# Kernel tuning notes

Hardware: AMD Instinct MI355X
Metric: run time of the kernel (lower is better)

The kernel has to match this reference:

```python
import jax, jax.numpy as jnp
import numpy as np

NUM_USERS = 100000
NUM_ITEMS = 50000
N_NODES = NUM_USERS + NUM_ITEMS
N_EDGES = 2_000_000
D = 64          # embedding_dim
HEADS = 4
F1 = D // HEADS  # per-head out dim of gat1
BATCH = 16384
NEG_SLOPE = 0.2  # PyG GATConv default negative_slope


def setup_inputs() -> dict:
    key = jax.random.key(0)
    ks = jax.random.split(key, 13)
    inp = {}
    inp["edge_index"] = jax.random.randint(ks[0], (2, N_EDGES), 0, N_NODES, dtype=jnp.int64)
    inp["batch_user_idx"] = jax.random.randint(ks[1], (BATCH,), 0, NUM_USERS, dtype=jnp.int64)
    inp["batch_item_idx"] = jax.random.randint(ks[2], (BATCH,), 0, NUM_ITEMS, dtype=jnp.int64)
    # Embedding tables (nn.init.normal_ std=0.01)
    inp["user_emb"] = 0.01 * jax.random.normal(ks[3], (NUM_USERS, D), dtype=jnp.float32)
    inp["item_emb"] = 0.01 * jax.random.normal(ks[4], (NUM_ITEMS, D), dtype=jnp.float32)
    # gat1: GATConv(64, 16, heads=4, concat=True)
    inp["W1"] = jax.random.normal(ks[5], (D, HEADS * F1), dtype=jnp.float32) / np.sqrt(D)
    inp["a_src1"] = jax.random.normal(ks[6], (HEADS, F1), dtype=jnp.float32) / np.sqrt(F1)
    inp["a_dst1"] = jax.random.normal(ks[7], (HEADS, F1), dtype=jnp.float32) / np.sqrt(F1)
    inp["b1"] = jnp.zeros((HEADS * F1,), dtype=jnp.float32)
    # gat2: GATConv(64, 64, heads=1)
    inp["W2"] = jax.random.normal(ks[8], (D, D), dtype=jnp.float32) / np.sqrt(D)
    inp["a_src2"] = jax.random.normal(ks[9], (1, D), dtype=jnp.float32) / np.sqrt(D)
    inp["a_dst2"] = jax.random.normal(ks[10], (1, D), dtype=jnp.float32) / np.sqrt(D)
    inp["b2"] = jnp.zeros((D,), dtype=jnp.float32)
    return inp


def _gat_conv(x, src, dst, W, a_src, a_dst, b, num_nodes):
    """PyG GATConv (eval mode, concat, self-loops already in src/dst)."""
    H, F = a_src.shape
    h = (x @ W).reshape(num_nodes, H, F)                 # [N,H,F]
    alpha_s = jnp.einsum('nhf,hf->nh', h, a_src)         # [N,H]
    alpha_d = jnp.einsum('nhf,hf->nh', h, a_dst)
    e = alpha_s[src] + alpha_d[dst]                      # [E,H]
    e = jax.nn.leaky_relu(e, NEG_SLOPE)
    # scatter-softmax over destination neighborhoods
    m = jax.ops.segment_max(e, dst, num_segments=num_nodes)   # [N,H]
    e = jnp.exp(e - m[dst])
    denom = jax.ops.segment_sum(e, dst, num_segments=num_nodes)
    alpha = e / denom[dst]                               # [E,H]
    msg = h[src] * alpha[:, :, None]                     # [E,H,F]
    agg = jax.ops.segment_sum(msg, dst, num_segments=num_nodes)  # [N,H,F]
    return agg.reshape(num_nodes, H * F) + b


def reference(user_emb, item_emb, W1, a_src1, a_dst1, b1,
              W2, a_src2, a_dst2, b2,
              edge_index, batch_user_idx, batch_item_idx):
    x = jnp.concatenate([user_emb, item_emb], axis=0)    # [N,D]
    n = x.shape[0]
    loop = jnp.arange(n, dtype=edge_index.dtype)          # add_self_loops=True
    src = jnp.concatenate([edge_index[0], loop])
    dst = jnp.concatenate([edge_index[1], loop])
    x = jax.nn.elu(_gat_conv(x, src, dst, W1, a_src1, a_dst1, b1, n))
    x = jax.nn.elu(_gat_conv(x, src, dst, W2, a_src2, a_dst2, b2, n))
    u = x[batch_user_idx]
    v = x[batch_item_idx + NUM_USERS]
    return jax.nn.sigmoid(jnp.sum(u * v, axis=1))        # [BATCH]
```

## Files before the change

kernel.cpp:

```cpp
#include <hip/hip_runtime.h>
#include <math.h>

#define SHIFT 8
#define NBMAX 1024
#define CAP   4096
#define TILE  4096
#define HSCALE 64.0f

typedef float v2f __attribute__((ext_vector_type(2)));
typedef short bf16x8 __attribute__((ext_vector_type(8)));
typedef float f32x4 __attribute__((ext_vector_type(4)));

__device__ __forceinline__ unsigned short f2bf(float f) {
    unsigned u = __float_as_uint(f);
    unsigned r = u + 0x7FFFu + ((u >> 16) & 1u);
    return (unsigned short)(r >> 16);
}
__device__ __forceinline__ unsigned pack2bf(float lo, float hi) {
    return (unsigned)f2bf(lo) | ((unsigned)f2bf(hi) << 16);
}
__device__ __forceinline__ float bflo(unsigned u) { return __uint_as_float(u << 16); }
__device__ __forceinline__ float bfhi(unsigned u) { return __uint_as_float(u & 0xFFFF0000u); }


__global__ void k_prep_w(const float* __restrict__ W1, const float* __restrict__ W2,
                         unsigned short* __restrict__ WT1, unsigned short* __restrict__ WT2,
                         unsigned* __restrict__ gcur, int NB) {
    int t = blockIdx.x * 256 + threadIdx.x;
    if (t < 4096) {
        int n = t & 63, k = t >> 6;
        WT1[n * 64 + k] = f2bf(W1[k * 64 + n]);
        WT2[n * 64 + k] = f2bf(W2[k * 64 + n]);
    }
    if (t < NB) gcur[t] = (unsigned)t * CAP;
}


__global__ __launch_bounds__(512) void k_partition(
    const int* __restrict__ src, const int* __restrict__ dst, int E,
    unsigned* __restrict__ gcur, unsigned* __restrict__ pairs, int NB) {
    __shared__ unsigned lh[NBMAX];
    __shared__ unsigned lcur[NBMAX];
    int t = threadIdx.x;
    for (int q = t; q < NB; q += 512) lh[q] = 0;
    __syncthreads();
    int base = blockIdx.x * TILE;
    int end = min(E, base + TILE);
    for (int i = base + t; i < end; i += 512)
        atomicAdd(&lh[((unsigned)dst[i]) >> SHIFT], 1u);
    __syncthreads();
    for (int q = t; q < NB; q += 512) {
        unsigned c = lh[q];
        lcur[q] = c ? atomicAdd(&gcur[q], c) : 0u;
    }
    __syncthreads();
    for (int i = base + t; i < end; i += 512) {
        unsigned d = (unsigned)dst[i];
        unsigned pos = atomicAdd(&lcur[d >> SHIFT], 1u);
        pairs[pos] = ((d & 255u) << 18) | (unsigned)src[i];
    }
}

__global__ __launch_bounds__(512) void k_bucket_sort(
    const unsigned* __restrict__ pairs, const unsigned* __restrict__ gcur,
    unsigned* __restrict__ beg, unsigned* __restrict__ endd,
    int* __restrict__ srt, int N, int NB) {
    __shared__ unsigned lh[256];
    __shared__ unsigned lcur[256];
    __shared__ unsigned sh[256];
    __shared__ int ssrt[CAP];
    int b = blockIdx.x;
    int t = threadIdx.x;
    unsigned s0 = (unsigned)b * CAP;
    int cnt = (int)(gcur[b] - s0);
    if (t < 256) lh[t] = 0;
    __syncthreads();
    for (int i = t; i < cnt; i += 512)
        atomicAdd(&lh[pairs[s0 + i] >> 18], 1u);
    __syncthreads();
    unsigned deg_t = 0;
    if (t < 256) { deg_t = lh[t]; sh[t] = deg_t; }
    __syncthreads();
    for (int off = 1; off < 256; off <<= 1) {
        unsigned x = 0;
        if (t < 256 && t >= off) x = sh[t - off];
        __syncthreads();
        if (t < 256) sh[t] += x;
        __syncthreads();
    }
    if (t < 256) {
        unsigned excl = sh[t] - deg_t;
        lcur[t] = excl;
        int node = (b << SHIFT) + t;
        if (node < N) { beg[node] = s0 + excl; endd[node] = s0 + excl + deg_t; }
    }
    __syncthreads();
    for (int i = t; i < cnt; i += 512) {
        unsigned pk = pairs[s0 + i];
        unsigned p = atomicAdd(&lcur[pk >> 18], 1u);
        ssrt[p] = (int)(pk & 0x3FFFFu);
    }
    __syncthreads();
    for (int i = t; i < cnt; i += 512) srt[s0 + i] = ssrt[i];
}


template <int HT, int BIN>
__global__ __launch_bounds__(256) void k_linear_mfma(
    const void* __restrict__ xav, const void* __restrict__ xbv, int split,
    const unsigned short* __restrict__ WTg,
    const float* __restrict__ a_src, const float* __restrict__ a_dst,
    unsigned char* __restrict__ h, float* __restrict__ as_out,
    float* __restrict__ ad_out, int N) {
    __shared__ unsigned short sX[64 * 72];
    __shared__ unsigned short sWT[64 * 72];
    __shared__ float sH[64 * 68];
    int t = threadIdx.x;
    int nodeBase = blockIdx.x * 64;

    {
        int r = t >> 2, c4 = (t & 3) * 16;
        int n = nodeBase + r;
        uint4 A = {0,0,0,0}, Bv = {0,0,0,0};
        if (BIN) {
            if (n < N) {
                const unsigned short* row = (const unsigned short*)xav + (size_t)n * 64 + c4;
                A  = ((const uint4*)(const void*)row)[0];
                Bv = ((const uint4*)(const void*)row)[1];
            }
        } else {
            float4 v0 = {0,0,0,0}, v1 = {0,0,0,0}, v2 = {0,0,0,0}, v3 = {0,0,0,0};
            if (n < N) {
                const float* row = (n < split) ? ((const float*)xav + (size_t)n * 64 + c4)
                                               : ((const float*)xbv + (size_t)(n - split) * 64 + c4);
                const float4* r4 = (const float4*)row;
                v0 = r4[0]; v1 = r4[1]; v2 = r4[2]; v3 = r4[3];
            }
            A  = make_uint4(pack2bf(v0.x, v0.y), pack2bf(v0.z, v0.w),
                            pack2bf(v1.x, v1.y), pack2bf(v1.z, v1.w));
            Bv = make_uint4(pack2bf(v2.x, v2.y), pack2bf(v2.z, v2.w),
                            pack2bf(v3.x, v3.y), pack2bf(v3.z, v3.w));
        }
        *(uint4*)(void*)(sX + r * 72 + c4) = A;
        *(uint4*)(void*)(sX + r * 72 + c4 + 8) = Bv;
        const uint4* wsrc = (const uint4*)(const void*)WTg;
        int base = (r * 64 + c4) >> 3;
        *(uint4*)(void*)(sWT + r * 72 + c4) = wsrc[base];
        *(uint4*)(void*)(sWT + r * 72 + c4 + 8) = wsrc[base + 1];
    }
    __syncthreads();

    {
        int lane = t & 63, w = t >> 6;
        int gl = lane & 15, quad = lane >> 4;
        int m0 = w * 16;
        const bf16x8 a0 = *(const bf16x8*)(void*)(sX + (m0 + gl) * 72 + quad * 8);
        const bf16x8 a1 = *(const bf16x8*)(void*)(sX + (m0 + gl) * 72 + 32 + quad * 8);
        f32x4 acc[4];
#pragma unroll
        for (int tt = 0; tt < 4; ++tt) {
            const bf16x8 b0 = *(const bf16x8*)(void*)(sWT + (tt * 16 + gl) * 72 + quad * 8);
            const bf16x8 b1 = *(const bf16x8*)(void*)(sWT + (tt * 16 + gl) * 72 + 32 + quad * 8);
            f32x4 c = {0.f, 0.f, 0.f, 0.f};
            c = __builtin_amdgcn_mfma_f32_16x16x32_bf16(a0, b0, c, 0, 0, 0);
            c = __builtin_amdgcn_mfma_f32_16x16x32_bf16(a1, b1, c, 0, 0, 0);
            acc[tt] = c;
        }
#pragma unroll
        for (int tt = 0; tt < 4; ++tt)
#pragma unroll
            for (int rr = 0; rr < 4; ++rr)
                sH[(m0 + quad * 4 + rr) * 68 + tt * 16 + gl] = acc[tt][rr];
    }
    __syncthreads();

    {
        int m = t >> 2, p = t & 3;
        int n = nodeBase + m;
        const float4* sp = (const float4*)(void*)(sH + m * 68 + p * 16);
        float4 q0 = sp[0], q1 = sp[1], q2 = sp[2], q3 = sp[3];
        float hv[16] = {q0.x,q0.y,q0.z,q0.w, q1.x,q1.y,q1.z,q1.w,
                        q2.x,q2.y,q2.z,q2.w, q3.x,q3.y,q3.z,q3.w};
        if (n < N) {
            unsigned dwords[4];
#pragma unroll
            for (int q = 0; q < 4; ++q) {
                int d0 = __builtin_amdgcn_cvt_pk_fp8_f32(hv[4*q] * HSCALE, hv[4*q+1] * HSCALE, 0, false);
                d0 = __builtin_amdgcn_cvt_pk_fp8_f32(hv[4*q+2] * HSCALE, hv[4*q+3] * HSCALE, d0, true);
                dwords[q] = (unsigned)d0;
            }
            ((uint4*)h)[(size_t)n * 4 + p] = make_uint4(dwords[0], dwords[1], dwords[2], dwords[3]);
            float ps = 0.f, pd = 0.f;
#pragma unroll
            for (int i = 0; i < 16; ++i) {
                ps = fmaf(hv[i], a_src[p * 16 + i], ps);
                pd = fmaf(hv[i], a_dst[p * 16 + i], pd);
            }
            if (HT == 4) {
                as_out[n * 4 + p] = ps;
                ad_out[n * 4 + p] = pd;
            } else {
                ps += __shfl_xor(ps, 1, 64); ps += __shfl_xor(ps, 2, 64);
                pd += __shfl_xor(pd, 1, 64); pd += __shfl_xor(pd, 2, 64);
                if (p == 0) { as_out[n] = ps; ad_out[n] = pd; }
            }
        }
    }
}

template <int HT>
__global__ __launch_bounds__(256, 4) void k_gat(
                      const int* __restrict__ srt, const unsigned* __restrict__ beg,
                      const unsigned* __restrict__ endd,
                      const unsigned* __restrict__ hq, const float* __restrict__ as,
                      const float* __restrict__ ad, const float* __restrict__ b,
                      unsigned* __restrict__ xout, int N) {
    int lane = threadIdx.x & 63;
    int wid = (int)((blockIdx.x * blockDim.x + threadIdx.x) >> 6);
    int gl = lane & 15;
    int d = wid * 4 + (lane >> 4);
    bool active = d < N;
    const int hh = (HT == 4) ? (gl >> 2) : 0;
    const int bb = (lane & 48) << 2;
    const int wb = bb + (hh << 4);
    const unsigned gl4 = (unsigned)gl << 2;
    const char* hqb = (const char*)hq;

    float adv = 0.f, l = 0.f;
    float a0 = 0.f, a1 = 0.f, a2 = 0.f, a3 = 0.f;
    int kb = 0, end = 0;
    if (active) {
        adv = ad[d * HT + hh];
        float e0 = as[d * HT + hh] + adv;
        e0 = (e0 > 0.f) ? e0 : 0.2f * e0;
        float w0 = __expf(e0);
        unsigned dw = hq[(size_t)d * 16 + gl];
        v2f lo = __builtin_amdgcn_cvt_pk_f32_fp8((int)dw, false);
        v2f hi = __builtin_amdgcn_cvt_pk_f32_fp8((int)dw, true);
        l = w0;
        a0 = w0 * lo.x; a1 = w0 * lo.y; a2 = w0 * hi.x; a3 = w0 * hi.y;
        kb = (int)beg[d];
        end = (int)endd[d];
    }

    while (__ballot(kb < end)) {
        int m = end - kb;
        int s_own = 0;
        if (gl < m) s_own = srt[kb + gl];

        float wq[4] = {0.f, 0.f, 0.f, 0.f};
        if (HT == 1) {
            if (gl < m) {
                float e = as[s_own] + adv;
                e = (e > 0.f) ? e : 0.2f * e;
                wq[0] = __expf(e);
            }
        } else {
            int eb = (gl & 3) << 2;
#pragma unroll
            for (int r = 0; r < 4; ++r) {
                int se = __builtin_amdgcn_ds_bpermute(bb + ((eb + r) << 2), s_own);
                if (eb + r < m) {
                    float e = as[(se << 2) + hh] + adv;
                    e = (e > 0.f) ? e : 0.2f * e;
                    wq[r] = __expf(e);
                }
            }
        }

        unsigned voff = ((unsigned)s_own) << 6;
        unsigned rr[16];
#pragma unroll
        for (int i = 0; i < 16; ++i) {
            unsigned vo = (unsigned)__builtin_amdgcn_ds_bpermute(bb + (i << 2), (int)voff);
            rr[i] = *(const unsigned*)(hqb + (vo + gl4));
        }

#pragma unroll
        for (int i = 0; i < 16; ++i) {
            float w;
            if (HT == 1) {
                w = __uint_as_float((unsigned)__builtin_amdgcn_ds_bpermute(
                        bb + (i << 2), (int)__float_as_uint(wq[0])));
            } else {
                w = __uint_as_float((unsigned)__builtin_amdgcn_ds_bpermute(
                        wb + ((i >> 2) << 2), (int)__float_as_uint(wq[i & 3])));
            }
            v2f lo = __builtin_amdgcn_cvt_pk_f32_fp8((int)rr[i], false);
            v2f hi = __builtin_amdgcn_cvt_pk_f32_fp8((int)rr[i], true);
            l += w;
            a0 = fmaf(w, lo.x, a0);
            a1 = fmaf(w, lo.y, a1);
            a2 = fmaf(w, hi.x, a2);
            a3 = fmaf(w, hi.y, a3);
        }
        kb += 16;
    }

    if (active) {
        float4 bb4 = ((const float4*)b)[gl];
        float rs = 1.f / (l * HSCALE);
        float v0 = a0 * rs + bb4.x;
        float v1 = a1 * rs + bb4.y;
        float v2 = a2 * rs + bb4.z;
        float v3 = a3 * rs + bb4.w;
        float o0 = (v0 > 0.f) ? v0 : expm1f(v0);
        float o1 = (v1 > 0.f) ? v1 : expm1f(v1);
        float o2 = (v2 > 0.f) ? v2 : expm1f(v2);
        float o3 = (v3 > 0.f) ? v3 : expm1f(v3);
        ((uint2*)xout)[(size_t)d * 16 + gl] = make_uint2(pack2bf(o0, o1), pack2bf(o2, o3));
    }
}

__global__ void k_dot_sig(const uint2* __restrict__ x2, const int* __restrict__ uidx,
                          const int* __restrict__ vidx, float* __restrict__ out,
                          int batch, int numUsers) {
    int lane = threadIdx.x & 63;
    int gl = lane & 15;
    int q = (int)(((blockIdx.x * blockDim.x + threadIdx.x) >> 6) * 4 + (lane >> 4));
    if (q >= batch) return;
    int u = uidx[q];
    int v = vidx[q] + numUsers;
    uint2 a = x2[(size_t)u * 16 + gl];
    uint2 c = x2[(size_t)v * 16 + gl];
    float p = bflo(a.x) * bflo(c.x) + bfhi(a.x) * bfhi(c.x)
            + bflo(a.y) * bflo(c.y) + bfhi(a.y) * bfhi(c.y);
#pragma unroll
    for (int off = 1; off < 16; off <<= 1) p += __shfl_xor(p, off, 64);
    if (gl == 0) out[q] = 1.f / (1.f + __expf(-p));
}


static inline int cdiv(long long a, long long b) { return (int)((a + b - 1) / b); }

extern "C" void kernel_launch(void* const* d_in, const int* in_sizes, int n_in,
                              void* d_out, int out_size, void* d_ws, size_t ws_size,
                              hipStream_t stream) {
    const int* edge_index = (const int*)d_in[0];
    const int* buidx      = (const int*)d_in[1];
    const int* biidx      = (const int*)d_in[2];
    const float* user_emb = (const float*)d_in[3];
    const float* item_emb = (const float*)d_in[4];
    const float* W1     = (const float*)d_in[5];
    const float* a_src1 = (const float*)d_in[6];
    const float* a_dst1 = (const float*)d_in[7];
    const float* b1     = (const float*)d_in[8];
    const float* W2     = (const float*)d_in[9];
    const float* a_src2 = (const float*)d_in[10];
    const float* a_dst2 = (const float*)d_in[11];
    const float* b2     = (const float*)d_in[12];
    float* out = (float*)d_out;

    const int E  = in_sizes[0] / 2;
    const int B  = in_sizes[1];
    const int NU = in_sizes[3] / 64;
    const int NI = in_sizes[4] / 64;
    const int N  = NU + NI;
    const int NB = cdiv(N, 1 << SHIFT);

    const int* src = edge_index;
    const int* dst = edge_index + E;

    float* ws = (float*)d_ws;
    size_t off = 0;
    unsigned* x_buf  = (unsigned*)(ws + off); off += (size_t)N * 32;
    unsigned* h_buf  = (unsigned*)(ws + off); off += (size_t)N * 16;
    float*    as_b   = ws + off; off += (size_t)N * 4;
    float*    ad_b   = ws + off; off += (size_t)N * 4;
    unsigned* gcur_b = (unsigned*)(ws + off); off += NBMAX;
    unsigned* beg_b  = (unsigned*)(ws + off); off += (size_t)N;
    unsigned* end_b  = (unsigned*)(ws + off); off += (size_t)N;
    unsigned* pairs_b= (unsigned*)(ws + off); off += (size_t)NB * CAP;
    int*      srt_b  = (int*)(ws + off); off += (size_t)NB * CAP;
    unsigned short* wt1_b = (unsigned short*)(ws + off); off += 2048;
    unsigned short* wt2_b = (unsigned short*)(ws + off); off += 2048;

    const int BS = 256;

    k_prep_w<<<16, BS, 0, stream>>>(W1, W2, wt1_b, wt2_b, gcur_b, NB);
    k_partition<<<cdiv(E, TILE), 512, 0, stream>>>(src, dst, E, gcur_b, pairs_b, NB);
    k_bucket_sort<<<NB, 512, 0, stream>>>(pairs_b, gcur_b, beg_b, end_b, srt_b, N, NB);

    k_linear_mfma<4, 0><<<cdiv(N, 64), BS, 0, stream>>>(user_emb, item_emb, NU, wt1_b,
                                                        a_src1, a_dst1,
                                                        (unsigned char*)h_buf, as_b, ad_b, N);
    k_gat<4><<<cdiv((long long)N * 16, BS), BS, 0, stream>>>(
        srt_b, beg_b, end_b, h_buf, as_b, ad_b, b1, x_buf, N);

    k_linear_mfma<1, 1><<<cdiv(N, 64), BS, 0, stream>>>(x_buf, x_buf, N, wt2_b,
                                                        a_src2, a_dst2,
                                                        (unsigned char*)h_buf, as_b, ad_b, N);
    k_gat<1><<<cdiv((long long)N * 16, BS), BS, 0, stream>>>(
        srt_b, beg_b, end_b, h_buf, as_b, ad_b, b2, x_buf, N);

    k_dot_sig<<<cdiv((long long)B * 16, BS), BS, 0, stream>>>(
        (const uint2*)x_buf, buidx, biidx, out, B, NU);
}
```

Before: 267.2 us.

## Process 32 neighbors per iteration via LDS broadcast instead of bpermute

```diff
diff --git a/kernel.cpp b/kernel.cpp
--- a/kernel.cpp
+++ b/kernel.cpp
@@ -215,16 +215,21 @@
                       const unsigned* __restrict__ hq, const float* __restrict__ as,
                       const float* __restrict__ ad, const float* __restrict__ b,
                       unsigned* __restrict__ xout, int N) {
-    int lane = threadIdx.x & 63;
-    int wid = (int)((blockIdx.x * blockDim.x + threadIdx.x) >> 6);
+    __shared__ unsigned s_vo[4][4][32];
+    __shared__ float    s_w[4][4][HT * 32];
+
+    int t = threadIdx.x;
+    int lane = t & 63;
+    int wv = t >> 6;
     int gl = lane & 15;
-    int d = wid * 4 + (lane >> 4);
+    int g  = lane >> 4;
+    int wid = (int)((blockIdx.x * blockDim.x + t) >> 6);
+    int d = wid * 4 + g;
     bool active = d < N;
     const int hh = (HT == 4) ? (gl >> 2) : 0;
-    const int bb = (lane & 48) << 2;
-    const int wb = bb + (hh << 4);
     const unsigned gl4 = (unsigned)gl << 2;
     const char* hqb = (const char*)hq;
+    const char* asb = (const char*)as;
 
     float adv = 0.f, l = 0.f;
     float a0 = 0.f, a1 = 0.f, a2 = 0.f, a3 = 0.f;
@@ -243,58 +248,122 @@
         end = (int)endd[d];
     }
 
-    while (__ballot(kb < end)) {
-        int m = end - kb;
-        int s_own = 0;
-        if (gl < m) s_own = srt[kb + gl];
-
-        float wq[4] = {0.f, 0.f, 0.f, 0.f};
+    int m = end - kb;
+    while (__ballot(m > 0)) {
+        unsigned v0 = 0, v1 = 0;
+        if (gl < m)      v0 = ((unsigned)srt[kb + gl]) << 6;
+        if (gl + 16 < m) v1 = ((unsigned)srt[kb + gl + 16]) << 6;
+
+        float w0 = 0.f, w1 = 0.f;
         if (HT == 1) {
+            float as0 = 0.f, as1 = 0.f;
+            if (gl < m)      as0 = *(const float*)(asb + (v0 >> 4));
+            if (gl + 16 < m) as1 = *(const float*)(asb + (v1 >> 4));
+            s_vo[wv][g][gl]      = v0;
+            s_vo[wv][g][gl + 16] = v1;
+            asm volatile("s_waitcnt lgkmcnt(0)" ::: "memory");
+            __builtin_amdgcn_sched_barrier(0);
+            unsigned rr[32];
+            const uint4* vob = (const uint4*)(const void*)&s_vo[wv][g][0];
+#pragma unroll
+            for (int c = 0; c < 8; ++c) {
+                uint4 vv = vob[c];
+                rr[4*c+0] = *(const unsigned*)(hqb + (vv.x + gl4));
+                rr[4*c+1] = *(const unsigned*)(hqb + (vv.y + gl4));
+                rr[4*c+2] = *(const unsigned*)(hqb + (vv.z + gl4));
+                rr[4*c+3] = *(const unsigned*)(hqb + (vv.w + gl4));
+            }
             if (gl < m) {
-                float e = as[s_own] + adv;
+                float e = as0 + adv;
                 e = (e > 0.f) ? e : 0.2f * e;
-                wq[0] = __expf(e);
+                w0 = __expf(e);
+            }
+            if (gl + 16 < m) {
+                float e = as1 + adv;
+                e = (e > 0.f) ? e : 0.2f * e;
+                w1 = __expf(e);
+            }
+            s_w[wv][g][gl]      = w0;
+            s_w[wv][g][gl + 16] = w1;
+            asm volatile("s_waitcnt lgkmcnt(0)" ::: "memory");
+            __builtin_amdgcn_sched_barrier(0);
+            const float4* wrd = (const float4*)(const void*)&s_w[wv][g][0];
+#pragma unroll
+            for (int c = 0; c < 8; ++c) {
+                float4 wc = wrd[c];
+                float wj[4] = {wc.x, wc.y, wc.z, wc.w};
+#pragma unroll
+                for (int j = 0; j < 4; ++j) {
+                    float w = wj[j];
+                    unsigned rv = rr[4*c + j];
+                    v2f lo = __builtin_amdgcn_cvt_pk_f32_fp8((int)rv, false);
+                    v2f hi = __builtin_amdgcn_cvt_pk_f32_fp8((int)rv, true);
+                    l += w;
+                    a0 = fmaf(w, lo.x, a0);
+                    a1 = fmaf(w, lo.y, a1);
+                    a2 = fmaf(w, hi.x, a2);
+                    a3 = fmaf(w, hi.y, a3);
+                }
             }
         } else {
-            int eb = (gl & 3) << 2;
-#pragma unroll
-            for (int r = 0; r < 4; ++r) {
-                int se = __builtin_amdgcn_ds_bpermute(bb + ((eb + r) << 2), s_own);
+            s_vo[wv][g][gl]      = v0;
+            s_vo[wv][g][gl + 16] = v1;
+            asm volatile("s_waitcnt lgkmcnt(0)" ::: "memory");
+            __builtin_amdgcn_sched_barrier(0);
+            int eb = (gl & 3) << 3;
+            const uint4* vop = (const uint4*)(const void*)&s_vo[wv][g][eb];
+            uint4 va = vop[0], vb = vop[1];
+            unsigned vs[8] = {va.x, va.y, va.z, va.w, vb.x, vb.y, vb.z, vb.w};
+            float av[8];
+#pragma unroll
+            for (int r = 0; r < 8; ++r)
+                av[r] = *(const float*)(asb + ((vs[r] >> 2) + ((unsigned)hh << 2)));
+            unsigned rr[32];
+            const uint4* vob = (const uint4*)(const void*)&s_vo[wv][g][0];
+#pragma unroll
+            for (int c = 0; c < 8; ++c) {
+                uint4 vv = vob[c];
+                rr[4*c+0] = *(const unsigned*)(hqb + (vv.x + gl4));
+                rr[4*c+1] = *(const unsigned*)(hqb + (vv.y + gl4));
+                rr[4*c+2] = *(const unsigned*)(hqb + (vv.z + gl4));
+                rr[4*c+3] = *(const unsigned*)(hqb + (vv.w + gl4));
+            }
+            float wq[8];
+#pragma unroll
+            for (int r = 0; r < 8; ++r) {
+                wq[r] = 0.f;
                 if (eb + r < m) {
-                    float e = as[(se << 2) + hh] + adv;
+                    float e = av[r] + adv;
                     e = (e > 0.f) ? e : 0.2f * e;
                     wq[r] = __expf(e);
                 }
             }
+            float4* wp = (float4*)(void*)&s_w[wv][g][hh * 32 + eb];
+            wp[0] = make_float4(wq[0], wq[1], wq[2], wq[3]);
+            wp[1] = make_float4(wq[4], wq[5], wq[6], wq[7]);
+            asm volatile("s_waitcnt lgkmcnt(0)" ::: "memory");
+            __builtin_amdgcn_sched_barrier(0);
+            const float4* wrd = (const float4*)(const void*)&s_w[wv][g][hh * 32];
+#pragma unroll
+            for (int c = 0; c < 8; ++c) {
+                float4 wc = wrd[c];
+                float wj[4] = {wc.x, wc.y, wc.z, wc.w};
+#pragma unroll
+                for (int j = 0; j < 4; ++j) {
+                    float w = wj[j];
+                    unsigned rv = rr[4*c + j];
+                    v2f lo = __builtin_amdgcn_cvt_pk_f32_fp8((int)rv, false);
+                    v2f hi = __builtin_amdgcn_cvt_pk_f32_fp8((int)rv, true);
+                    l += w;
+                    a0 = fmaf(w, lo.x, a0);
+                    a1 = fmaf(w, lo.y, a1);
+                    a2 = fmaf(w, hi.x, a2);
+                    a3 = fmaf(w, hi.y, a3);
+                }
+            }
         }
-
-        unsigned voff = ((unsigned)s_own) << 6;
-        unsigned rr[16];
-#pragma unroll
-        for (int i = 0; i < 16; ++i) {
-            unsigned vo = (unsigned)__builtin_amdgcn_ds_bpermute(bb + (i << 2), (int)voff);
-            rr[i] = *(const unsigned*)(hqb + (vo + gl4));
-        }
-
-#pragma unroll
-        for (int i = 0; i < 16; ++i) {
-            float w;
-            if (HT == 1) {
-                w = __uint_as_float((unsigned)__builtin_amdgcn_ds_bpermute(
-                        bb + (i << 2), (int)__float_as_uint(wq[0])));
-            } else {
-                w = __uint_as_float((unsigned)__builtin_amdgcn_ds_bpermute(
-                        wb + ((i >> 2) << 2), (int)__float_as_uint(wq[i & 3])));
-            }
-            v2f lo = __builtin_amdgcn_cvt_pk_f32_fp8((int)rr[i], false);
-            v2f hi = __builtin_amdgcn_cvt_pk_f32_fp8((int)rr[i], true);
-            l += w;
-            a0 = fmaf(w, lo.x, a0);
-            a1 = fmaf(w, lo.y, a1);
-            a2 = fmaf(w, hi.x, a2);
-            a3 = fmaf(w, hi.y, a3);
-        }
-        kb += 16;
+        kb += 32;
+        m = end - kb;
     }
 
     if (active) {
```

After: 255.4 us. 1.05x faster.
